# Performance work log

Measured on AMD Instinct MI355X. Metric: run time of the kernel, lower is better.

The kernel has to match this reference:

```python
import jax, jax.numpy as jnp
import numpy as np

B, Q, C, K = 2, 300, 80, 300
MH = MW = 128
TH = TW = 320


def setup_inputs() -> dict:
    key = jax.random.key(0)
    k1, k2, k3 = jax.random.split(key, 3)
    pred_logits = jax.random.normal(k1, (B, Q, C), dtype=jnp.float32)
    pred_boxes = jax.random.uniform(k2, (B, Q, 4), dtype=jnp.float32)  # cxcywh in [0,1]
    pred_masks = jax.random.normal(k3, (B, Q, MH, MW), dtype=jnp.float32)
    # fixed target size so resize output shape is static (original uses .item() per image)
    orig_target_sizes = jnp.full((B, 2), 320.0, dtype=jnp.float32)  # (w, h)
    return {
        'pred_logits': pred_logits,
        'pred_boxes': pred_boxes,
        'pred_masks': pred_masks,
        'orig_target_sizes': orig_target_sizes,
        'target_h': TH,
        'target_w': TW,
    }


def reference(pred_logits, pred_boxes, pred_masks, orig_target_sizes, target_h, target_w):
    b, q, c = pred_logits.shape
    # cxcywh -> xyxy
    cx, cy, w, h = jnp.split(pred_boxes, 4, axis=-1)
    boxes_xyxy = jnp.concatenate([cx - 0.5 * w, cy - 0.5 * h, cx + 0.5 * w, cy + 0.5 * h], axis=-1)
    # scale factor [w, h, w, h] per image
    scale_fct = jnp.concatenate([orig_target_sizes, orig_target_sizes], axis=1)[:, None, :]  # [B,1,4]
    boxes_abs = boxes_xyxy * scale_fct  # [B,Q,4]

    # focal-loss path: sigmoid scores, topk over flattened (query, class)
    scores_flat = jax.nn.sigmoid(pred_logits).reshape(b, q * c)
    scores, index_flat = jax.lax.top_k(scores_flat, K)  # [B,K]
    labels = index_flat % c
    query_indices = index_flat // c  # [B,K]

    top_boxes = jnp.take_along_axis(boxes_abs, query_indices[:, :, None], axis=1)  # [B,K,4]
    top_masks = jnp.take_along_axis(pred_masks, query_indices[:, :, None, None], axis=1)  # [B,K,MH,MW]

    # bilinear resize, half-pixel centers == torch align_corners=False
    resized = jax.image.resize(top_masks, (b, K, target_h, target_w), method='linear')
    binary_masks = (jax.nn.sigmoid(resized) > 0.5).astype(jnp.float32)

    return scores, labels, top_boxes, binary_masks
```

## Files before the change

kernel.cpp:

```cpp
#include <hip/hip_runtime.h>
#include <stdint.h>

constexpr int Bq = 2;
constexpr int Qn = 300;
constexpr int Cn = 80;
constexpr int Kn = 300;
constexpr int NFLAT = Qn * Cn;
constexpr int MHs = 128;
constexpr int MWs = 128;
constexpr int THs = 320;
constexpr int TWs = 320;

constexpr int OFF_SCORES = 0;
constexpr int OFF_LABELS = Bq * Kn;
constexpr int OFF_BOXES  = 2 * Bq * Kn;
constexpr int OFF_MASKS  = 2 * Bq * Kn + Bq * Kn * 4;

constexpr int TPB = 1024;
constexpr int EPT = (NFLAT + TPB - 1) / TPB;

typedef float vf4  __attribute__((ext_vector_type(4)));
typedef float uvf4 __attribute__((ext_vector_type(4), aligned(4)));

__global__ __launch_bounds__(TPB) void topk_kernel(
    const float* __restrict__ logits,
    const float* __restrict__ boxes,
    const float* __restrict__ osz,
    float* __restrict__ out,
    int* __restrict__ qidx_ws)
{
    const int b    = blockIdx.x;
    const int tid  = threadIdx.x;
    const int wave = tid >> 6;
    const float* lg = logits + (size_t)b * NFLAT;

    uint32_t key[EPT];
    #pragma unroll
    for (int j = 0; j < EPT; ++j) {
        int idx = j * TPB + tid;
        bool valid = (idx < NFLAT);
        float x = valid ? lg[idx] : 0.0f;
        float s = 1.0f / (1.0f + expf(-x));
        key[j] = valid ? __float_as_uint(s) : 0u;
    }

    __shared__ int cnt[2][16];
    __shared__ int sh_cnt;
    __shared__ unsigned long long sk[1024];
    if (tid == 0) sh_cnt = 0;

    uint32_t lo = 0u, hi = 0x3F800000u;
    for (int it = 0; it < 32 && (hi - lo) > 1u; ++it) {
        const uint32_t mid = lo + ((hi - lo) >> 1);
        int c = 0;
        #pragma unroll
        for (int j = 0; j < EPT; ++j) c += (key[j] > mid) ? 1 : 0;
        #pragma unroll
        for (int off = 32; off > 0; off >>= 1) c += __shfl_down(c, off);
        if ((tid & 63) == 0) cnt[it & 1][wave] = c;
        __syncthreads();
        int total = 0;
        #pragma unroll
        for (int w = 0; w < 16; ++w) total += cnt[it & 1][w];
        if (total >= Kn) { lo = mid; if (total <= 768) break; }
        else             { hi = mid; }
    }

    const uint32_t T = lo;
    #pragma unroll
    for (int j = 0; j < EPT; ++j) {
        int idx = j * TPB + tid;
        if (idx < NFLAT && key[j] > T) {
            int p = atomicAdd(&sh_cnt, 1);
            if (p < 1024)
                sk[p] = ((unsigned long long)key[j] << 32)
                      | (unsigned long long)(0xFFFFFFFFu - (uint32_t)idx);
        }
    }
    __syncthreads();

    const int n = min(sh_cnt, 1024);
    if (tid < n) {
        unsigned long long my = sk[tid];
        int rank = 0;
        for (int i = 0; i < n; ++i) rank += (sk[i] > my) ? 1 : 0;
        if (rank < Kn) {
            uint32_t idx = 0xFFFFFFFFu - (uint32_t)(my & 0xFFFFFFFFull);
            float score  = __uint_as_float((uint32_t)(my >> 32));
            int label = (int)(idx % (uint32_t)Cn);
            int q     = (int)(idx / (uint32_t)Cn);

            out[OFF_SCORES + b * Kn + rank] = score;
            out[OFF_LABELS + b * Kn + rank] = (float)label;

            const float sw = osz[b * 2 + 0];
            const float sh = osz[b * 2 + 1];
            const float* bx = boxes + ((size_t)(b * Qn + q)) * 4;
            float cx = bx[0], cy = bx[1], w = bx[2], h = bx[3];
            float* ob = out + OFF_BOXES + ((size_t)(b * Kn + rank)) * 4;
            ob[0] = (cx - 0.5f * w) * sw;
            ob[1] = (cy - 0.5f * h) * sh;
            ob[2] = (cx + 0.5f * w) * sw;
            ob[3] = (cy + 0.5f * h) * sh;

            qidx_ws[b * Kn + rank] = q;
        }
    }
}

__global__ __launch_bounds__(320) void resize_kernel(
    const float* __restrict__ masks,
    const int* __restrict__ qidx_ws,
    float* __restrict__ out)
{
    const int blk = blockIdx.x;
    const int bk  = blk >> 2;
    const int s   = blk & 3;
    const int tid = threadIdx.x;
    const int b   = bk / Kn;
    const int q   = qidx_ws[bk];
    const int c   = tid % 80;
    const int rs  = tid / 80;

    const float* M = masks + ((size_t)(b * Qn + q)) * (MHs * MWs);

    int s0;
    {
        float sx0 = fmaf(0.4f, (float)(4 * c), -0.3f);
        int i0 = (int)floorf(sx0);
        s0 = min(max(i0, 0), MWs - 4);
    }
    float W[4][4];
    #pragma unroll
    for (int t = 0; t < 4; ++t) {
        int ox = 4 * c + t;
        float sx = fmaf(0.4f, (float)ox, -0.3f);
        int ix0 = (int)floorf(sx);
        float fr = sx - (float)ix0;
        int ca = max(ix0, 0);
        int cb = min(ix0 + 1, MWs - 1);
        float wa = 1.0f - fr, wb = fr;
        #pragma unroll
        for (int j = 0; j < 4; ++j) {
            float w = 0.0f;
            if (s0 + j == ca) w += wa;
            if (s0 + j == cb) w += wb;
            W[t][j] = w;
        }
    }

    auto hrow = [&](float* hv, int r) {
        uvf4 a = *(const uvf4*)(M + r * MWs + s0);
        #pragma unroll
        for (int t = 0; t < 4; ++t)
            hv[t] = fmaf(W[t][0], a[0],
                    fmaf(W[t][1], a[1],
                    fmaf(W[t][2], a[2], W[t][3] * a[3])));
    };

    float* outm = out + OFF_MASKS + (size_t)bk * (THs * TWs);
    auto emit = [&](int row, float wA, const float* pA, float wB, const float* pB) {
        vf4 o;
        #pragma unroll
        for (int t = 0; t < 4; ++t) {
            float v = fmaf(wA, pA[t], wB * pB[t]);
            o[t] = (v > 0.0f) ? 1.0f : 0.0f;
        }
        __builtin_nontemporal_store(o, (vf4*)(outm + (size_t)row * TWs + 4 * c));
    };

    const int Y0 = 80 * s + 20 * rs;
    const int M0 = Y0 / 5;

    float hA[4], hB[4], hC[4], hD[4];
    hrow(hC, max(2 * M0 - 1, 0));
    hrow(hD, 2 * M0);

    #pragma unroll
    for (int g = 0; g < 4; ++g) {
        #pragma unroll
        for (int t = 0; t < 4; ++t) { hA[t] = hC[t]; hB[t] = hD[t]; }
        const int Mg = M0 + g;
        hrow(hC, 2 * Mg + 1);
        hrow(hD, min(2 * Mg + 2, MHs - 1));

        const int Y = Y0 + 5 * g;
        emit(Y + 0, 0.3f, hA, 0.7f, hB);
        emit(Y + 1, 0.9f, hB, 0.1f, hC);
        emit(Y + 2, 0.5f, hB, 0.5f, hC);
        emit(Y + 3, 0.1f, hB, 0.9f, hC);
        emit(Y + 4, 0.7f, hC, 0.3f, hD);
    }
}

extern "C" void kernel_launch(void* const* d_in, const int* in_sizes, int n_in,
                              void* d_out, int out_size, void* d_ws, size_t ws_size,
                              hipStream_t stream) {
    const float* logits = (const float*)d_in[0];
    const float* boxes  = (const float*)d_in[1];
    const float* masks  = (const float*)d_in[2];
    const float* osz    = (const float*)d_in[3];

    float* out = (float*)d_out;
    int* qidx  = (int*)d_ws;

    topk_kernel<<<Bq, TPB, 0, stream>>>(logits, boxes, osz, out, qidx);
    resize_kernel<<<Bq * Kn * 4, 320, 0, stream>>>(masks, qidx, out);
}
```

Baseline: 326.2 us.

## Use 4-way threshold search, wave-aggregated compaction, and halve resize grid

The top-k threshold search now tests three pivots per iteration, so each pass cuts the range into quarters. The three counts are packed into one 64-bit value for a single shuffle reduction, which roughly halves the number of block-wide barriers. Candidate compaction uses a ballot plus one atomic per wave instead of one atomic per element. The resize kernel now covers two row strips per block and launches half as many blocks, cutting per-block overhead at the cost of fewer blocks in flight.

```diff
diff --git a/kernel.cpp b/kernel.cpp
--- a/kernel.cpp
+++ b/kernel.cpp
@@ -32,6 +32,7 @@
     const int b    = blockIdx.x;
     const int tid  = threadIdx.x;
     const int wave = tid >> 6;
+    const int lane = tid & 63;
     const float* lg = logits + (size_t)b * NFLAT;
 
     uint32_t key[EPT];
@@ -44,34 +45,54 @@
         key[j] = valid ? __float_as_uint(s) : 0u;
     }
 
-    __shared__ int cnt[2][16];
+    __shared__ unsigned long long cnt3[2][16];
     __shared__ int sh_cnt;
     __shared__ unsigned long long sk[1024];
     if (tid == 0) sh_cnt = 0;
 
     uint32_t lo = 0u, hi = 0x3F800000u;
-    for (int it = 0; it < 32 && (hi - lo) > 1u; ++it) {
-        const uint32_t mid = lo + ((hi - lo) >> 1);
-        int c = 0;
-        #pragma unroll
-        for (int j = 0; j < EPT; ++j) c += (key[j] > mid) ? 1 : 0;
-        #pragma unroll
-        for (int off = 32; off > 0; off >>= 1) c += __shfl_down(c, off);
-        if ((tid & 63) == 0) cnt[it & 1][wave] = c;
+    for (int it = 0; it < 16; ++it) {
+        if (hi - lo <= 3u) break;
+        const uint32_t step = (hi - lo) >> 2;
+        const uint32_t m1 = lo + step, m2 = lo + 2 * step, m3 = lo + 3 * step;
+        int c1 = 0, c2 = 0, c3 = 0;
+        #pragma unroll
+        for (int j = 0; j < EPT; ++j) {
+            uint32_t k = key[j];
+            c1 += (k > m1) ? 1 : 0;
+            c2 += (k > m2) ? 1 : 0;
+            c3 += (k > m3) ? 1 : 0;
+        }
+        unsigned long long p = (unsigned long long)c1
+                             | ((unsigned long long)c2 << 16)
+                             | ((unsigned long long)c3 << 32);
+        #pragma unroll
+        for (int off = 32; off > 0; off >>= 1) p += __shfl_down(p, off);
+        if (lane == 0) cnt3[it & 1][wave] = p;
         __syncthreads();
-        int total = 0;
-        #pragma unroll
-        for (int w = 0; w < 16; ++w) total += cnt[it & 1][w];
-        if (total >= Kn) { lo = mid; if (total <= 768) break; }
-        else             { hi = mid; }
+        unsigned long long tot = 0;
+        #pragma unroll
+        for (int w = 0; w < 16; ++w) tot += cnt3[it & 1][w];
+        const int n1 = (int)(tot & 0xFFFFull);
+        const int n2 = (int)((tot >> 16) & 0xFFFFull);
+        const int n3 = (int)((tot >> 32) & 0xFFFFull);
+        if (n3 >= Kn)      { lo = m3;          if (n3 <= 768) break; }
+        else if (n2 >= Kn) { lo = m2; hi = m3; if (n2 <= 768) break; }
+        else if (n1 >= Kn) { lo = m1; hi = m2; if (n1 <= 768) break; }
+        else               { hi = m1; }
     }
 
     const uint32_t T = lo;
     #pragma unroll
     for (int j = 0; j < EPT; ++j) {
         int idx = j * TPB + tid;
-        if (idx < NFLAT && key[j] > T) {
-            int p = atomicAdd(&sh_cnt, 1);
+        bool pred = (idx < NFLAT) && (key[j] > T);
+        unsigned long long m = __ballot(pred);
+        int base = 0;
+        if (lane == 0 && m) base = atomicAdd(&sh_cnt, __popcll(m));
+        base = __shfl(base, 0);
+        if (pred) {
+            int p = base + __popcll(m & ((1ull << lane) - 1ull));
             if (p < 1024)
                 sk[p] = ((unsigned long long)key[j] << 32)
                       | (unsigned long long)(0xFFFFFFFFu - (uint32_t)idx);
@@ -114,8 +135,8 @@
     float* __restrict__ out)
 {
     const int blk = blockIdx.x;
-    const int bk  = blk >> 2;
-    const int s   = blk & 3;
+    const int bk  = blk >> 1;
+    const int sP  = (blk & 1) * 2;
     const int tid = threadIdx.x;
     const int b   = bk / Kn;
     const int q   = qidx_ws[bk];
@@ -169,27 +190,31 @@
         __builtin_nontemporal_store(o, (vf4*)(outm + (size_t)row * TWs + 4 * c));
     };
 
-    const int Y0 = 80 * s + 20 * rs;
-    const int M0 = Y0 / 5;
-
-    float hA[4], hB[4], hC[4], hD[4];
-    hrow(hC, max(2 * M0 - 1, 0));
-    hrow(hD, 2 * M0);
-
-    #pragma unroll
-    for (int g = 0; g < 4; ++g) {
-        #pragma unroll
-        for (int t = 0; t < 4; ++t) { hA[t] = hC[t]; hB[t] = hD[t]; }
-        const int Mg = M0 + g;
-        hrow(hC, 2 * Mg + 1);
-        hrow(hD, min(2 * Mg + 2, MHs - 1));
-
-        const int Y = Y0 + 5 * g;
-        emit(Y + 0, 0.3f, hA, 0.7f, hB);
-        emit(Y + 1, 0.9f, hB, 0.1f, hC);
-        emit(Y + 2, 0.5f, hB, 0.5f, hC);
-        emit(Y + 3, 0.1f, hB, 0.9f, hC);
-        emit(Y + 4, 0.7f, hC, 0.3f, hD);
+    #pragma unroll
+    for (int sc = 0; sc < 2; ++sc) {
+        const int s  = sP + sc;
+        const int Y0 = 80 * s + 20 * rs;
+        const int M0 = Y0 / 5;
+
+        float hA[4], hB[4], hC[4], hD[4];
+        hrow(hC, max(2 * M0 - 1, 0));
+        hrow(hD, 2 * M0);
+
+        #pragma unroll
+        for (int g = 0; g < 4; ++g) {
+            #pragma unroll
+            for (int t = 0; t < 4; ++t) { hA[t] = hC[t]; hB[t] = hD[t]; }
+            const int Mg = M0 + g;
+            hrow(hC, 2 * Mg + 1);
+            hrow(hD, min(2 * Mg + 2, MHs - 1));
+
+            const int Y = Y0 + 5 * g;
+            emit(Y + 0, 0.3f, hA, 0.7f, hB);
+            emit(Y + 1, 0.9f, hB, 0.1f, hC);
+            emit(Y + 2, 0.5f, hB, 0.5f, hC);
+            emit(Y + 3, 0.1f, hB, 0.9f, hC);
+            emit(Y + 4, 0.7f, hC, 0.3f, hD);
+        }
     }
 }
 
@@ -205,5 +230,5 @@
     int* qidx  = (int*)d_ws;
 
     topk_kernel<<<Bq, TPB, 0, stream>>>(logits, boxes, osz, out, qidx);
-    resize_kernel<<<Bq * Kn * 4, 320, 0, stream>>>(masks, qidx, out);
+    resize_kernel<<<Bq * Kn * 2, 320, 0, stream>>>(masks, qidx, out);
 }
```

Result: no change. 319.9 us (-1.9%).
